# Kernel optimization log

Measured on AMD Instinct MI355X. Metric: run time of the kernel, lower is better.

Reference implementation:

```python
import jax, jax.numpy as jnp
import numpy as np

B, C, H, W = 4, 256, 64, 64
RC = 32  # reduced channels = C // reduction


def setup_inputs() -> dict:
    key = jax.random.key(0)
    ks = jax.random.split(key, 5)
    return {
        "x": jax.random.normal(ks[0], (B, C, H, W), dtype=jnp.float32),
        "context": jax.random.normal(ks[1], (B, C, H, W), dtype=jnp.float32),
        "Wq": jax.random.normal(ks[2], (RC, C), dtype=jnp.float32) * 0.02,
        "bq": jnp.zeros((RC,), dtype=jnp.float32),
        "Wk": jax.random.normal(ks[3], (RC, C), dtype=jnp.float32) * 0.02,
        "bk": jnp.zeros((RC,), dtype=jnp.float32),
        "Wv": jax.random.normal(ks[4], (C, C), dtype=jnp.float32) * 0.02,
        "bv": jnp.zeros((C,), dtype=jnp.float32),
        "gamma": jnp.ones((1,), dtype=jnp.float32),
    }


def reference(x, context, Wq, bq, Wk, bk, Wv, bv, gamma):
    b, c, h, w = x.shape
    _, _, hc, wc = context.shape
    n, m = h * w, hc * wc
    xf = x.reshape(b, c, n)          # (B,C,N)
    cf = context.reshape(b, c, m)    # (B,C,M)
    # 1x1 conv projections == per-pixel linear
    q = jnp.einsum('rc,bcn->bnr', Wq, xf) + bq            # (B,N,RC)
    k = jnp.einsum('rc,bcm->brm', Wk, cf) + bk[:, None]   # (B,RC,M)
    v = jnp.einsum('dc,bcm->bdm', Wv, cf) + bv[:, None]   # (B,C,M)
    scale = 1.0 / jnp.sqrt(jnp.asarray(q.shape[-1], dtype=q.dtype))
    attn = jax.nn.softmax(jnp.einsum('bnr,brm->bnm', q, k) * scale, axis=-1)  # (B,N,M)
    out = jnp.einsum('bdm,bnm->bdn', v, attn).reshape(b, c, h, w)
    return gamma * out + x
```

## Files before the change

kernel.cpp:

```cpp
#include <hip/hip_runtime.h>
#include <hip/hip_bf16.h>


#define B_ 4
#define C_ 256
#define N_ 4096
#define M_ 4096
#define SCALE_ 0.17677669529663687f

typedef __bf16 bf16x8 __attribute__((ext_vector_type(8)));
typedef float f32x4 __attribute__((ext_vector_type(4)));
typedef float f32x16 __attribute__((ext_vector_type(16)));
typedef int i32x8 __attribute__((ext_vector_type(8)));

#define AS1 __attribute__((address_space(1)))
#define AS3 __attribute__((address_space(3)))

static __device__ __forceinline__ unsigned short f2bf(float f) {
    unsigned int u = __float_as_uint(f);
    return (unsigned short)((u + 0x7fffu + ((u >> 16) & 1u)) >> 16);
}
static __device__ __forceinline__ unsigned bfpk(float a, float b) {
    return (unsigned)f2bf(a) | ((unsigned)f2bf(b) << 16);
}
static __device__ __forceinline__ float fp8d(unsigned v) {
    unsigned e = (v >> 3) & 15, m = v & 7;
    float f = e ? __uint_as_float(((e + 120u) << 23) | (m << 20))
                : (float)m * 0x1p-9f;
    return (v & 0x80u) ? -f : f;
}

__global__ __launch_bounds__(256) void prep(
        const float* __restrict__ Wq, const float* __restrict__ Wk,
        const float* __restrict__ Wv, uint4* __restrict__ Wqf,
        uint4* __restrict__ Wkf, uint4* __restrict__ Wvf) {
    int bid = blockIdx.x, t = threadIdx.x;
    const float* W;
    uint4* dst;
    int frag;
    if (bid < 32)      { W = Wv; dst = Wvf; frag = (bid * 256 + t) >> 6; }
    else if (bid < 36) { W = Wq; dst = Wqf; frag = ((bid - 32) * 256 + t) >> 6; }
    else               { W = Wk; dst = Wkf; frag = ((bid - 36) * 256 + t) >> 6; }
    int lane = t & 63, low = lane & 15, q = lane >> 4;
    int fch = frag & 7, fr = frag >> 3;
    const float* wp = W + (size_t)(fr * 16 + low) * C_ + fch * 32 + q * 8;
    float4 w0 = *(const float4*)wp;
    float4 w1 = *(const float4*)(wp + 4);
    uint4 pk = {bfpk(w0.x, w0.y), bfpk(w0.z, w0.w),
                bfpk(w1.x, w1.y), bfpk(w1.z, w1.w)};
    dst[(size_t)frag * 64 + lane] = pk;
}

__global__ __launch_bounds__(256, 2) void fused_proj(
        const float* __restrict__ x, const float* __restrict__ ctx,
        const uint4* __restrict__ Wqf, const uint4* __restrict__ Wkf,
        const uint4* __restrict__ Wvf,
        const float* __restrict__ bq, const float* __restrict__ bk,
        const float* __restrict__ bv,
        unsigned short* __restrict__ Qf, unsigned short* __restrict__ Kf,
        unsigned char* __restrict__ Vf) {
    __shared__ unsigned short X[64][264];
    __shared__ unsigned short Pl[4][16 * 40];
    __shared__ unsigned char  Vw[4][16 * 40];

    int bid = blockIdx.x;
    bool isX = bid >= 256;
    int lb = bid & 255;
    int b = lb >> 6, pt64 = lb & 63;
    const float* __restrict__ in = (isX ? x : ctx) + (size_t)b * C_ * N_ + pt64 * 64;
    int t = threadIdx.x, wg = t >> 6, lane = t & 63;
    int low = lane & 15, q = lane >> 4;

    {
        int pL = lane;
        const float* s0 = in + pL;
#pragma unroll
        for (int ct = 0; ct < 4; ct++) {
            const float* s2 = s0 + (size_t)(ct * 64 + wg * 16) * N_;
            float v[16];
#pragma unroll
            for (int k = 0; k < 16; k++) v[k] = s2[(size_t)k * N_];
#pragma unroll
            for (int k = 0; k < 16; k += 2)
                *(unsigned*)&X[pL][ct * 64 + wg * 16 + k] = bfpk(v[k], v[k + 1]);
        }
    }
    __syncthreads();

    {
        const uint4* __restrict__ Wf = isX ? Wqf : Wkf;
        const float* __restrict__ bias = isX ? bq : bk;
        unsigned short* __restrict__ dst = isX ? Qf : Kf;
        bf16x8 xf[8];
#pragma unroll
        for (int ch = 0; ch < 8; ch++)
            xf[ch] = *(const bf16x8*)&X[wg * 16 + low][ch * 32 + q * 8];
        const f32x4 zero = {0.f, 0.f, 0.f, 0.f};
        f32x4 acc[2] = {zero, zero};
#pragma unroll
        for (int rt = 0; rt < 2; rt++)
#pragma unroll
            for (int ch = 0; ch < 8; ch++) {
                uint4 wv = Wf[(rt * 8 + ch) * 64 + lane];
                acc[rt] = __builtin_amdgcn_mfma_f32_16x16x32_bf16(
                    __builtin_bit_cast(bf16x8, wv), xf[ch], acc[rt], 0, 0, 0);
            }
        unsigned short* Pw = &Pl[wg][0];
#pragma unroll
        for (int rt = 0; rt < 2; rt++) {
            float b0 = bias[rt * 16 + q * 4 + 0], b1 = bias[rt * 16 + q * 4 + 1];
            float b2 = bias[rt * 16 + q * 4 + 2], b3 = bias[rt * 16 + q * 4 + 3];
            uint2 pk = {bfpk(acc[rt][0] + b0, acc[rt][1] + b1),
                        bfpk(acc[rt][2] + b2, acc[rt][3] + b3)};
            *(uint2*)(Pw + low * 40 + rt * 16 + q * 4) = pk;
        }
        uint4 frag = *(const uint4*)(Pw + low * 40 + q * 8);
        ((uint4*)dst)[((size_t)b * 256 + pt64 * 4 + wg) * 64 + lane] = frag;
    }

    if (!isX) {
        int mstep = wg >> 1, dh = wg & 1;
        bf16x8 vfr[2][8];
#pragma unroll
        for (int mt = 0; mt < 2; mt++)
#pragma unroll
            for (int ch = 0; ch < 8; ch++)
                vfr[mt][ch] = *(const bf16x8*)&X[mstep * 32 + mt * 16 + low][ch * 32 + q * 8];
        unsigned char* Vv = &Vw[wg][0];
        int msg = pt64 * 2 + mstep;
        const f32x4 zero = {0.f, 0.f, 0.f, 0.f};
#pragma unroll
        for (int dt8 = 0; dt8 < 8; dt8++) {
            int dt = dh * 8 + dt8;
            f32x4 a0 = zero, a1 = zero;
#pragma unroll
            for (int ch = 0; ch < 8; ch++) {
                uint4 wv = Wvf[(dt * 8 + ch) * 64 + lane];
                bf16x8 wfr = __builtin_bit_cast(bf16x8, wv);
                a0 = __builtin_amdgcn_mfma_f32_16x16x32_bf16(vfr[0][ch], wfr, a0, 0, 0, 0);
                a1 = __builtin_amdgcn_mfma_f32_16x16x32_bf16(vfr[1][ch], wfr, a1, 0, 0, 0);
            }
            float bb = bv[dt * 16 + low];
            unsigned w0 = __builtin_amdgcn_cvt_pk_fp8_f32(a0[0] + bb, a0[1] + bb, 0, false);
            w0 = __builtin_amdgcn_cvt_pk_fp8_f32(a0[2] + bb, a0[3] + bb, w0, true);
            unsigned w1 = __builtin_amdgcn_cvt_pk_fp8_f32(a1[0] + bb, a1[1] + bb, 0, false);
            w1 = __builtin_amdgcn_cvt_pk_fp8_f32(a1[2] + bb, a1[3] + bb, w1, true);
            *(unsigned*)(Vv + low * 40 + q * 4) = w0;
            *(unsigned*)(Vv + low * 40 + 16 + q * 4) = w1;
            uint2 fr = *(const uint2*)(Vv + low * 40 + q * 8);
            ((uint2*)Vf)[(((size_t)b * 128 + msg) * 16 + dt) * 64 + lane] = fr;
        }
    }
}

__global__ __launch_bounds__(256, 3) void attn(
        const unsigned short* __restrict__ Qf, const unsigned short* __restrict__ Kf,
        const unsigned char* __restrict__ Vf, unsigned char* __restrict__ Op,
        float* __restrict__ Lp) {
    __shared__ __align__(16) unsigned char Pb[2][4][16 * 80];
    __shared__ __align__(16) unsigned Odw[64 * 68];

    int bid = blockIdx.x;
    int v = bid >> 6;
    int ng = bid & 63;
    int b = v / 3;
    int chunk = v - b * 3;
    int I  = (chunk == 0) ? 22 : 21;
    int s0 = (chunk == 0) ? 0 : (chunk == 1 ? 22 : 43);

    int wave = threadIdx.x >> 6, lane = threadIdx.x & 63;
    int q = lane >> 4, low = lane & 15;
    int hi = lane >> 5;
    int dsel = q & 1;
    int nt = ng * 4 + wave;

    const uint4* Qp = (const uint4*)Qf;
    const uint4* Kp = (const uint4*)Kf + (size_t)b * 256 * 64;
    const uint2* Vq = (const uint2*)(Vf + (size_t)b * 1048576) + (size_t)hi * 1024 + low;

    bf16x8 qa = __builtin_bit_cast(bf16x8, Qp[(size_t)(b * 256 + nt) * 64 + lane]);

    f32x16 acc2[2][2];
#pragma unroll
    for (int tp = 0; tp < 2; tp++)
#pragma unroll
        for (int dg = 0; dg < 2; dg++) acc2[tp][dg] = (f32x16)(0.f);
    float lacc = 0.f;
    const f32x4 zero = {0.f, 0.f, 0.f, 0.f};

    uint4 kv[4];
#pragma unroll
    for (int u = 0; u < 4; u++)
        kv[u] = Kp[(size_t)(s0 * 4 + u) * 64 + lane];
    f32x4 s[4];
#pragma unroll
    for (int u = 0; u < 4; u++)
        s[u] = __builtin_amdgcn_mfma_f32_16x16x32_bf16(
            __builtin_bit_cast(bf16x8, kv[u]), qa, zero, 0, 0, 0);
    if (I > 1) {
#pragma unroll
        for (int u = 0; u < 4; u++)
            kv[u] = Kp[(size_t)((s0 + 1) * 4 + u) * 64 + lane];
    }
    {
        unsigned char* Pw = &Pb[0][wave][0];
#pragma unroll
        for (int u = 0; u < 4; u++) {
            float p0 = __expf(s[u][0] * SCALE_), p1 = __expf(s[u][1] * SCALE_);
            float p2 = __expf(s[u][2] * SCALE_), p3 = __expf(s[u][3] * SCALE_);
            lacc += p0 + p1 + p2 + p3;
            unsigned w = __builtin_amdgcn_cvt_pk_fp8_f32(p0, p1, 0, false);
            w = __builtin_amdgcn_cvt_pk_fp8_f32(p2, p3, w, true);
            *(unsigned*)(Pw + low * 80 + u * 16 + q * 4) = w;
        }
    }
    __syncthreads();

    for (int i = 0; i < I; i++) {
        int cur = i & 1, nxt = cur ^ 1;

        i32x8 vf[2];
        {
            const uint2* Vs = Vq + (size_t)(s0 + i) * 2048;
#pragma unroll
            for (int dg = 0; dg < 2; dg++) {
                int dt = wave * 4 + dg * 2 + dsel;
                long* dqw = (long*)&vf[dg];
#pragma unroll
                for (int ss = 0; ss < 4; ss++)
                    dqw[ss] = *(const long*)(Vs + dt * 64 + ss * 16);
            }
        }

        if (i + 1 < I) {
#pragma unroll
            for (int u = 0; u < 4; u++)
                s[u] = __builtin_amdgcn_mfma_f32_16x16x32_bf16(
                    __builtin_bit_cast(bf16x8, kv[u]), qa, zero, 0, 0, 0);
            if (i + 2 < I) {
#pragma unroll
                for (int u = 0; u < 4; u++)
                    kv[u] = Kp[(size_t)((s0 + i + 2) * 4 + u) * 64 + lane];
            }
        }

        const unsigned char* Pr = &Pb[cur][0][0];
        __builtin_amdgcn_s_setprio(1);
#pragma unroll
        for (int tp = 0; tp < 2; tp++) {
            const unsigned char* pr = Pr + (tp * 2 + dsel) * 1280 + low * 80 + hi * 32;
            i32x8 pf;
            ((uint4*)&pf)[0] = *(const uint4*)pr;
            ((uint4*)&pf)[1] = *(const uint4*)(pr + 16);
#pragma unroll
            for (int dg = 0; dg < 2; dg++)
                acc2[tp][dg] = __builtin_amdgcn_mfma_scale_f32_32x32x64_f8f6f4(
                    vf[dg], pf, acc2[tp][dg], 0, 0, 0, 127, 0, 127);
        }
        __builtin_amdgcn_s_setprio(0);

        if (i + 1 < I) {
            unsigned char* Pw = &Pb[nxt][wave][0];
#pragma unroll
            for (int u = 0; u < 4; u++) {
                float p0 = __expf(s[u][0] * SCALE_), p1 = __expf(s[u][1] * SCALE_);
                float p2 = __expf(s[u][2] * SCALE_), p3 = __expf(s[u][3] * SCALE_);
                lacc += p0 + p1 + p2 + p3;
                unsigned w = __builtin_amdgcn_cvt_pk_fp8_f32(p0, p1, 0, false);
                w = __builtin_amdgcn_cvt_pk_fp8_f32(p2, p3, w, true);
                *(unsigned*)(Pw + low * 80 + u * 16 + q * 4) = w;
            }
        }
        __syncthreads();
    }

    lacc += __shfl_xor(lacc, 16, 64);
    lacc += __shfl_xor(lacc, 32, 64);
    if (lane < 16)
        Lp[(size_t)v * 4096 + nt * 16 + lane] = lacc;

    int l31 = lane & 31;
#pragma unroll
    for (int tp = 0; tp < 2; tp++)
#pragma unroll
        for (int dg = 0; dg < 2; dg++)
#pragma unroll
            for (int k = 0; k < 4; k++) {
                unsigned w = __builtin_amdgcn_cvt_pk_fp8_f32(
                    acc2[tp][dg][4 * k + 0], acc2[tp][dg][4 * k + 1], 0, false);
                w = __builtin_amdgcn_cvt_pk_fp8_f32(
                    acc2[tp][dg][4 * k + 2], acc2[tp][dg][4 * k + 3], w, true);
                Odw[(tp * 32 + l31) * 68 + wave * 16 + dg * 8 + k * 2 + hi] = w;
            }
    __syncthreads();
    {
        int n = threadIdx.x >> 2, c4 = threadIdx.x & 3;
        size_t rb = ((size_t)v * 4096 + ng * 64 + n) * 256;
#pragma unroll
        for (int k = 0; k < 4; k++)
            *(uint4*)(Op + rb + c4 * 64 + k * 16) =
                *(const uint4*)&Odw[n * 68 + c4 * 16 + k * 4];
    }
}

__global__ __launch_bounds__(256) void combine(
        const unsigned char* __restrict__ Op, const float* __restrict__ Lp,
        const float* __restrict__ x, const float* __restrict__ gamma,
        float* __restrict__ out) {
    __shared__ float W[32][260];
    int bid = blockIdx.x;
    int b = bid >> 7, n0 = (bid & 127) * 32;
    int t = threadIdx.x;
    float g = gamma[0];
    {
        int d4 = t & 63, nn = t >> 6;
#pragma unroll
        for (int rr = 0; rr < 8; rr++) {
            int n = rr * 4 + nn;
            float o0 = 0.f, o1 = 0.f, o2 = 0.f, o3 = 0.f, l = 0.f;
#pragma unroll
            for (int p = 0; p < 3; p++) {
                size_t base = (size_t)(b * 3 + p) * 4096 + n0 + n;
                unsigned pv = *(const unsigned*)(Op + base * 256 + d4 * 4);
                o0 += fp8d(pv & 255u); o1 += fp8d((pv >> 8) & 255u);
                o2 += fp8d((pv >> 16) & 255u); o3 += fp8d(pv >> 24);
                l += Lp[base];
            }
            float sc = g / l;
            f32x4 w = {o0 * sc, o1 * sc, o2 * sc, o3 * sc};
            *(f32x4*)&W[n][d4 * 4] = w;
        }
    }
    __syncthreads();
    {
        int d = t;
        size_t rb = ((size_t)b * 256 + d) * 4096 + n0;
#pragma unroll
        for (int k = 0; k < 8; k++) {
            f32x4 xv = *(const f32x4*)(x + rb + k * 4);
            f32x4 res;
#pragma unroll
            for (int r = 0; r < 4; r++) res[r] = W[k * 4 + r][d] + xv[r];
            *(f32x4*)(out + rb + k * 4) = res;
        }
    }
}

extern "C" void kernel_launch(void* const* d_in, const int* in_sizes, int n_in,
                              void* d_out, int out_size, void* d_ws, size_t ws_size,
                              hipStream_t stream) {
    const float* x     = (const float*)d_in[0];
    const float* ctx   = (const float*)d_in[1];
    const float* Wq    = (const float*)d_in[2];
    const float* bq    = (const float*)d_in[3];
    const float* Wk    = (const float*)d_in[4];
    const float* bk    = (const float*)d_in[5];
    const float* Wv    = (const float*)d_in[6];
    const float* bv    = (const float*)d_in[7];
    const float* gamma = (const float*)d_in[8];
    float* out = (float*)d_out;

    unsigned short* Qf = (unsigned short*)d_ws;
    unsigned short* Kf = Qf + (size_t)B_ * N_ * 32;
    unsigned char*  Vf = (unsigned char*)(Kf + (size_t)B_ * M_ * 32);
    uint4* Wqf = (uint4*)(Vf + (size_t)B_ * M_ * C_);
    uint4* Wkf = Wqf + 16 * 64;
    uint4* Wvf = Wkf + 16 * 64;
    unsigned char* Op = (unsigned char*)(Wvf + 128 * 64);
    float* Lp = (float*)(Op + (size_t)3 * B_ * N_ * C_);

    prep<<<40, 256, 0, stream>>>(Wq, Wk, Wv, Wqf, Wkf, Wvf);
    fused_proj<<<512, 256, 0, stream>>>(x, ctx, Wqf, Wkf, Wvf, bq, bk, bv, Qf, Kf, Vf);
    attn<<<768, 256, 0, stream>>>(Qf, Kf, Vf, Op, Lp);
    combine<<<512, 256, 0, stream>>>(Op, Lp, x, gamma, out);
}
```

Measured before the change: 150.1 us.

## Fuse combine into attention, drop split-M partials, use 512-thread blocks

Removes the three-way split of the key dimension and the separate combine kernel. Each 512-thread block now walks all 64 key chunks and normalises with gamma/l. It adds the residual x and writes the final output directly, so the fp8 partial-output round trip through global memory goes away. Four waves compute QK^T and softmax probabilities while all eight waves do the PV MFMAs, and the next V fragment is prefetched one step ahead. The grid shrinks to 256 blocks with a block index mapping meant to keep batch data on the same XCD, which risks lower parallelism and a longer serial loop per block.

After: 139.6 us. 7.0% less time.

```diff
diff --git a/kernel.cpp b/kernel.cpp
--- a/kernel.cpp
+++ b/kernel.cpp
@@ -22,12 +22,6 @@
 }
 static __device__ __forceinline__ unsigned bfpk(float a, float b) {
     return (unsigned)f2bf(a) | ((unsigned)f2bf(b) << 16);
-}
-static __device__ __forceinline__ float fp8d(unsigned v) {
-    unsigned e = (v >> 3) & 15, m = v & 7;
-    float f = e ? __uint_as_float(((e + 120u) << 23) | (m << 20))
-                : (float)m * 0x1p-9f;
-    return (v & 0x80u) ? -f : f;
 }
 
 __global__ __launch_bounds__(256) void prep(
@@ -153,56 +147,54 @@
     }
 }
 
-__global__ __launch_bounds__(256, 3) void attn(
+__global__ __launch_bounds__(512, 2) void attn(
         const unsigned short* __restrict__ Qf, const unsigned short* __restrict__ Kf,
-        const unsigned char* __restrict__ Vf, unsigned char* __restrict__ Op,
-        float* __restrict__ Lp) {
+        const unsigned char* __restrict__ Vf, const float* __restrict__ x,
+        const float* __restrict__ gamma, float* __restrict__ out) {
     __shared__ __align__(16) unsigned char Pb[2][4][16 * 80];
-    __shared__ __align__(16) unsigned Odw[64 * 68];
+    __shared__ float l_sh[64];
+    __shared__ unsigned Ot[64 * 129];
 
     int bid = blockIdx.x;
-    int v = bid >> 6;
-    int ng = bid & 63;
-    int b = v / 3;
-    int chunk = v - b * 3;
-    int I  = (chunk == 0) ? 22 : 21;
-    int s0 = (chunk == 0) ? 0 : (chunk == 1 ? 22 : 43);
+    int xcd = bid & 7, tq = bid >> 3;
+    int b = xcd >> 1;
+    int g = ((xcd & 1) << 5) + tq;
 
     int wave = threadIdx.x >> 6, lane = threadIdx.x & 63;
     int q = lane >> 4, low = lane & 15;
     int hi = lane >> 5;
     int dsel = q & 1;
-    int nt = ng * 4 + wave;
+    int l31 = lane & 31;
+    bool isQK = wave < 4;
 
     const uint4* Qp = (const uint4*)Qf;
     const uint4* Kp = (const uint4*)Kf + (size_t)b * 256 * 64;
     const uint2* Vq = (const uint2*)(Vf + (size_t)b * 1048576) + (size_t)hi * 1024 + low;
-
-    bf16x8 qa = __builtin_bit_cast(bf16x8, Qp[(size_t)(b * 256 + nt) * 64 + lane]);
-
-    f32x16 acc2[2][2];
-#pragma unroll
-    for (int tp = 0; tp < 2; tp++)
-#pragma unroll
-        for (int dg = 0; dg < 2; dg++) acc2[tp][dg] = (f32x16)(0.f);
+    int dt = wave * 2 + dsel;
+
+    bf16x8 qa;
+    if (isQK)
+        qa = __builtin_bit_cast(bf16x8, Qp[(size_t)(b * 256 + g * 4 + wave) * 64 + lane]);
+
+    f32x16 acc2[2];
+    acc2[0] = (f32x16)(0.f);
+    acc2[1] = (f32x16)(0.f);
     float lacc = 0.f;
     const f32x4 zero = {0.f, 0.f, 0.f, 0.f};
 
     uint4 kv[4];
-#pragma unroll
-    for (int u = 0; u < 4; u++)
-        kv[u] = Kp[(size_t)(s0 * 4 + u) * 64 + lane];
     f32x4 s[4];
-#pragma unroll
-    for (int u = 0; u < 4; u++)
-        s[u] = __builtin_amdgcn_mfma_f32_16x16x32_bf16(
-            __builtin_bit_cast(bf16x8, kv[u]), qa, zero, 0, 0, 0);
-    if (I > 1) {
+    if (isQK) {
 #pragma unroll
         for (int u = 0; u < 4; u++)
-            kv[u] = Kp[(size_t)((s0 + 1) * 4 + u) * 64 + lane];
-    }
-    {
+            kv[u] = Kp[(size_t)u * 64 + lane];
+#pragma unroll
+        for (int u = 0; u < 4; u++)
+            s[u] = __builtin_amdgcn_mfma_f32_16x16x32_bf16(
+                __builtin_bit_cast(bf16x8, kv[u]), qa, zero, 0, 0, 0);
+#pragma unroll
+        for (int u = 0; u < 4; u++)
+            kv[u] = Kp[(size_t)(4 + u) * 64 + lane];
         unsigned char* Pw = &Pb[0][wave][0];
 #pragma unroll
         for (int u = 0; u < 4; u++) {
@@ -214,33 +206,38 @@
             *(unsigned*)(Pw + low * 80 + u * 16 + q * 4) = w;
         }
     }
+    i32x8 vfc;
+    {
+        const uint2* Vs = Vq + (size_t)dt * 64;
+        long* dqw = (long*)&vfc;
+#pragma unroll
+        for (int ss = 0; ss < 4; ss++)
+            dqw[ss] = *(const long*)(Vs + ss * 16);
+    }
     __syncthreads();
 
-    for (int i = 0; i < I; i++) {
+    for (int i = 0; i < 64; i++) {
         int cur = i & 1, nxt = cur ^ 1;
-
-        i32x8 vf[2];
-        {
-            const uint2* Vs = Vq + (size_t)(s0 + i) * 2048;
-#pragma unroll
-            for (int dg = 0; dg < 2; dg++) {
-                int dt = wave * 4 + dg * 2 + dsel;
-                long* dqw = (long*)&vf[dg];
-#pragma unroll
-                for (int ss = 0; ss < 4; ss++)
-                    dqw[ss] = *(const long*)(Vs + dt * 64 + ss * 16);
-            }
-        }
-
-        if (i + 1 < I) {
+        bool haveNext = (i + 1 < 64);
+
+        i32x8 vfn;
+        if (haveNext) {
+            const uint2* Vs = Vq + (size_t)(i + 1) * 2048 + dt * 64;
+            long* dqw = (long*)&vfn;
+#pragma unroll
+            for (int ss = 0; ss < 4; ss++)
+                dqw[ss] = *(const long*)(Vs + ss * 16);
+        }
+
+        if (isQK && haveNext) {
 #pragma unroll
             for (int u = 0; u < 4; u++)
                 s[u] = __builtin_amdgcn_mfma_f32_16x16x32_bf16(
                     __builtin_bit_cast(bf16x8, kv[u]), qa, zero, 0, 0, 0);
-            if (i + 2 < I) {
+            if (i + 2 < 64) {
 #pragma unroll
                 for (int u = 0; u < 4; u++)
-                    kv[u] = Kp[(size_t)((s0 + i + 2) * 4 + u) * 64 + lane];
+                    kv[u] = Kp[(size_t)((i + 2) * 4 + u) * 64 + lane];
             }
         }
 
@@ -252,14 +249,12 @@
             i32x8 pf;
             ((uint4*)&pf)[0] = *(const uint4*)pr;
             ((uint4*)&pf)[1] = *(const uint4*)(pr + 16);
-#pragma unroll
-            for (int dg = 0; dg < 2; dg++)
-                acc2[tp][dg] = __builtin_amdgcn_mfma_scale_f32_32x32x64_f8f6f4(
-                    vf[dg], pf, acc2[tp][dg], 0, 0, 0, 127, 0, 127);
+            acc2[tp] = __builtin_amdgcn_mfma_scale_f32_32x32x64_f8f6f4(
+                vfc, pf, acc2[tp], 0, 0, 0, 127, 0, 127);
         }
         __builtin_amdgcn_s_setprio(0);
 
-        if (i + 1 < I) {
+        if (isQK && haveNext) {
             unsigned char* Pw = &Pb[nxt][wave][0];
 #pragma unroll
             for (int u = 0; u < 4; u++) {
@@ -271,77 +266,37 @@
                 *(unsigned*)(Pw + low * 80 + u * 16 + q * 4) = w;
             }
         }
+        if (haveNext) vfc = vfn;
         __syncthreads();
     }
 
-    lacc += __shfl_xor(lacc, 16, 64);
-    lacc += __shfl_xor(lacc, 32, 64);
-    if (lane < 16)
-        Lp[(size_t)v * 4096 + nt * 16 + lane] = lacc;
-
-    int l31 = lane & 31;
+    if (isQK) {
+        lacc += __shfl_xor(lacc, 16, 64);
+        lacc += __shfl_xor(lacc, 32, 64);
+        if (lane < 16)
+            l_sh[wave * 16 + low] = lacc;
+    }
+
 #pragma unroll
     for (int tp = 0; tp < 2; tp++)
 #pragma unroll
-        for (int dg = 0; dg < 2; dg++)
-#pragma unroll
-            for (int k = 0; k < 4; k++) {
-                unsigned w = __builtin_amdgcn_cvt_pk_fp8_f32(
-                    acc2[tp][dg][4 * k + 0], acc2[tp][dg][4 * k + 1], 0, false);
-                w = __builtin_amdgcn_cvt_pk_fp8_f32(
-                    acc2[tp][dg][4 * k + 2], acc2[tp][dg][4 * k + 3], w, true);
-                Odw[(tp * 32 + l31) * 68 + wave * 16 + dg * 8 + k * 2 + hi] = w;
-            }
+        for (int r = 0; r < 16; r += 2) {
+            int col16 = wave * 16 + ((r >> 1) & 1) + 4 * (r >> 2) + 2 * hi;
+            Ot[(tp * 32 + l31) * 129 + col16] = bfpk(acc2[tp][r], acc2[tp][r + 1]);
+        }
     __syncthreads();
+
     {
-        int n = threadIdx.x >> 2, c4 = threadIdx.x & 3;
-        size_t rb = ((size_t)v * 4096 + ng * 64 + n) * 256;
-#pragma unroll
-        for (int k = 0; k < 4; k++)
-            *(uint4*)(Op + rb + c4 * 64 + k * 16) =
-                *(const uint4*)&Odw[n * 68 + c4 * 16 + k * 4];
-    }
-}
-
-__global__ __launch_bounds__(256) void combine(
-        const unsigned char* __restrict__ Op, const float* __restrict__ Lp,
-        const float* __restrict__ x, const float* __restrict__ gamma,
-        float* __restrict__ out) {
-    __shared__ float W[32][260];
-    int bid = blockIdx.x;
-    int b = bid >> 7, n0 = (bid & 127) * 32;
-    int t = threadIdx.x;
-    float g = gamma[0];
-    {
-        int d4 = t & 63, nn = t >> 6;
-#pragma unroll
-        for (int rr = 0; rr < 8; rr++) {
-            int n = rr * 4 + nn;
-            float o0 = 0.f, o1 = 0.f, o2 = 0.f, o3 = 0.f, l = 0.f;
-#pragma unroll
-            for (int p = 0; p < 3; p++) {
-                size_t base = (size_t)(b * 3 + p) * 4096 + n0 + n;
-                unsigned pv = *(const unsigned*)(Op + base * 256 + d4 * 4);
-                o0 += fp8d(pv & 255u); o1 += fp8d((pv >> 8) & 255u);
-                o2 += fp8d((pv >> 16) & 255u); o3 += fp8d(pv >> 24);
-                l += Lp[base];
-            }
-            float sc = g / l;
-            f32x4 w = {o0 * sc, o1 * sc, o2 * sc, o3 * sc};
-            *(f32x4*)&W[n][d4 * 4] = w;
-        }
-    }
-    __syncthreads();
-    {
-        int d = t;
-        size_t rb = ((size_t)b * 256 + d) * 4096 + n0;
-#pragma unroll
-        for (int k = 0; k < 8; k++) {
-            f32x4 xv = *(const f32x4*)(x + rb + k * 4);
-            f32x4 res;
-#pragma unroll
-            for (int r = 0; r < 4; r++) res[r] = W[k * 4 + r][d] + xv[r];
-            *(f32x4*)(out + rb + k * 4) = res;
+        float gm = gamma[0];
+        float rinv = gm / l_sh[lane];
+        size_t nb = ((size_t)(b * 256 + wave * 32)) * 4096 + g * 64 + lane;
+#pragma unroll 4
+        for (int j = 0; j < 32; j++) {
+            unsigned pk = Ot[lane * 129 + wave * 16 + (j >> 1)];
+            unsigned bits = (j & 1) ? (pk & 0xffff0000u) : (pk << 16);
+            float o = __uint_as_float(bits);
+            size_t idx = nb + (size_t)j * 4096;
+            out[idx] = o * rinv + x[idx];
         }
     }
 }
@@ -366,11 +321,8 @@
     uint4* Wqf = (uint4*)(Vf + (size_t)B_ * M_ * C_);
     uint4* Wkf = Wqf + 16 * 64;
     uint4* Wvf = Wkf + 16 * 64;
-    unsigned char* Op = (unsigned char*)(Wvf + 128 * 64);
-    float* Lp = (float*)(Op + (size_t)3 * B_ * N_ * C_);
 
     prep<<<40, 256, 0, stream>>>(Wq, Wk, Wv, Wqf, Wkf, Wvf);
     fused_proj<<<512, 256, 0, stream>>>(x, ctx, Wqf, Wkf, Wvf, bq, bk, bv, Qf, Kf, Vf);
-    attn<<<768, 256, 0, stream>>>(Qf, Kf, Vf, Op, Lp);
-    combine<<<512, 256, 0, stream>>>(Op, Lp, x, gamma, out);
-}
+    attn<<<256, 512, 0, stream>>>(Qf, Kf, Vf, x, gamma, out);
+}
```
